# Optimization experiments

Measured on AMD Instinct MI355X. Metric: run time of the kernel, lower is better.

Reference implementation:

```python
import jax, jax.numpy as jnp
import numpy as np

B, T, C, H = 2, 2048, 1024, 16
D = C // H  # head dim = 64

def setup_inputs() -> dict:
    key = jax.random.key(0)
    k1, k2 = jax.random.split(key)
    x = jax.random.normal(k1, (B, T, C), dtype=jnp.float32)
    W_attn = jax.random.normal(k2, (3 * C, C), dtype=jnp.float32) * 0.02
    return {"x": x, "W_attn": W_attn}

def reference(x, W_attn):
    Bx, Tx, Cx = x.shape
    qkv = jnp.einsum('btc,fc->btf', x, W_attn)  # fused QKV projection (bias=False)
    q, k, v = jnp.split(qkv, 3, axis=-1)
    # [B, H, T, D]
    q = q.reshape(Bx, Tx, H, D).transpose(0, 2, 1, 3)
    k = k.reshape(Bx, Tx, H, D).transpose(0, 2, 1, 3)
    v = v.reshape(Bx, Tx, H, D).transpose(0, 2, 1, 3)
    scale = 1.0 / jnp.sqrt(jnp.asarray(D, dtype=q.dtype))
    scores = jnp.einsum('bhqd,bhkd->bhqk', q, k) * scale  # [B,H,T,T]
    causal = jnp.tril(jnp.ones((Tx, Tx), dtype=bool))
    scores = jnp.where(causal[None, None], scores, jnp.asarray(-jnp.inf, dtype=scores.dtype))
    attn = jax.nn.softmax(scores, axis=-1)
    y = jnp.einsum('bhqk,bhkd->bhqd', attn, v)
    y = y.transpose(0, 2, 1, 3).reshape(Bx, Tx, Cx)  # merge heads; dropout=0 at eval
    return y
```

## Files before the change

### kernel.cpp

```cpp
#include <hip/hip_runtime.h>
#include <hip/hip_bf16.h>

#define Bn 2
#define Tn 2048
#define Cn 1024
#define Hn 16
#define Dn 64
#define Mdim 4096
#define Ndim 3072
#define Kdim 1024

typedef unsigned short u16;
typedef __attribute__((ext_vector_type(8))) short bf16x8;
typedef __attribute__((ext_vector_type(4))) float f32x4;

__device__ __forceinline__ u16 f2bf(float v) {
    unsigned int x = __builtin_bit_cast(unsigned int, v);
    unsigned int r = (x + 0x7fffu + ((x >> 16) & 1u)) >> 16;
    return (u16)r;
}

__device__ __forceinline__ unsigned int pack2(float a, float b) {
    return (unsigned int)f2bf(a) | ((unsigned int)f2bf(b) << 16);
}

__device__ __forceinline__ unsigned int cvt_pk_bf16(float lo, float hi) {
    unsigned int r;
    asm("v_cvt_pk_bf16_f32 %0, %1, %2" : "=v"(r) : "v"(lo), "v"(hi));
    return r;
}

__device__ __forceinline__ void async16(const void* g, void* l) {
    __builtin_amdgcn_global_load_lds(
        (const __attribute__((address_space(1))) void*)g,
        (__attribute__((address_space(3))) void*)(unsigned int)(unsigned long long)l,
        16, 0, 0);
}

__device__ __forceinline__ int probe_inline(const unsigned int* __restrict__ X, int tid) {
    const int lane = tid & 63;
    int cnt = 0;
    #pragma unroll
    for (int i = 0; i < 8; i++) {
        unsigned int e = (X[lane * 8 + i] >> 7) & 0xFFu;
        cnt += (e >= 100u && e < 134u) ? 1 : 0;
    }
    #pragma unroll
    for (int off = 1; off < 64; off <<= 1) cnt += __shfl_xor(cnt, off);
    return cnt > 256 ? 1 : 0;
}

#define NXC ((size_t)Mdim * Kdim / 8)
#define NWC ((size_t)Ndim * Kdim / 8)

__global__ __launch_bounds__(256) void convert_in(
        const void* __restrict__ Xv, const void* __restrict__ Wv,
        u16* __restrict__ Xb, u16* __restrict__ Wb, int* __restrict__ flag) {
    const int isbf = probe_inline((const unsigned int*)Xv, threadIdx.x);
    if (blockIdx.x == 0 && threadIdx.x == 0) *flag = isbf;
    size_t i = (size_t)blockIdx.x * 256 + threadIdx.x;
    if (i >= NXC + NWC) return;
    const void* src; u16* dst; size_t off;
    if (i < NXC) { src = Xv; dst = Xb; off = i; }
    else         { src = Wv; dst = Wb; off = i - NXC; }
    if (isbf) {
        ((uint4*)dst)[off] = ((const uint4*)src)[off];
    } else {
        const float4* s = (const float4*)src + off * 2;
        float4 a = s[0], b = s[1];
        ((uint4*)dst)[off] = (uint4){pack2(a.x, a.y), pack2(a.z, a.w),
                                     pack2(b.x, b.y), pack2(b.z, b.w)};
    }
}

#define NTq (Kdim / 64)

#define PBAR() do { asm volatile("" ::: "memory"); \
                    __builtin_amdgcn_s_barrier();  \
                    asm volatile("" ::: "memory"); } while (0)
#define VMW(n) asm volatile("s_waitcnt vmcnt(" #n ")" ::: "memory")

#define QSTAGE_A(QIDX, BUF, KOFF) \
    async16(Xb + (size_t)(m0 + (QIDX) * 64 + srow) * Kdim + (KOFF) + gc, \
            &sA[BUF][(QIDX) * 4096 + w * 512])
#define QSTAGE_B(QIDX, BUF, KOFF) \
    async16(Wb + (size_t)(n0 + (QIDX) * 64 + srow) * Kdim + (KOFF) + gc, \
            &sB[BUF][(QIDX) * 4096 + w * 512])

#define RDA(MQ, BUF) do {                                                  \
    _Pragma("unroll")                                                      \
    for (int mt = 0; mt < 4; mt++) {                                       \
        const u16* p = &sA[BUF][(wm + (MQ) * 64 + mt * 16 + r16) * 64];    \
        af[mt][0] = *(const bf16x8*)(p + cx0);                             \
        af[mt][1] = *(const bf16x8*)(p + (cx0 ^ 32));                      \
    } } while (0)

#define RDB(NQ, BUF) do {                                                  \
    _Pragma("unroll")                                                      \
    for (int nt = 0; nt < 2; nt++) {                                       \
        const u16* p = &sB[BUF][(wn + (NQ) * 32 + nt * 16 + r16) * 64];    \
        bf[NQ][nt][0] = *(const bf16x8*)(p + cx0);                         \
        bf[NQ][nt][1] = *(const bf16x8*)(p + (cx0 ^ 32));                  \
    } } while (0)

#define MM(MQ, NQ) do {                                                    \
    __builtin_amdgcn_s_setprio(1);                                         \
    _Pragma("unroll")                                                      \
    for (int mt = 0; mt < 4; mt++)                                         \
        _Pragma("unroll")                                                  \
        for (int nt = 0; nt < 2; nt++) {                                   \
            acc[(MQ)*4+mt][(NQ)*2+nt] = __builtin_amdgcn_mfma_f32_16x16x32_bf16( \
                af[mt][0], bf[NQ][nt][0], acc[(MQ)*4+mt][(NQ)*2+nt], 0,0,0);     \
            acc[(MQ)*4+mt][(NQ)*2+nt] = __builtin_amdgcn_mfma_f32_16x16x32_bf16( \
                af[mt][1], bf[NQ][nt][1], acc[(MQ)*4+mt][(NQ)*2+nt], 0,0,0);     \
        }                                                                  \
    __builtin_amdgcn_s_setprio(0);                                         \
} while (0)

__global__ __launch_bounds__(512, 2) void qkv_gemm(
        const u16* __restrict__ Xb, const u16* __restrict__ Wb,
        u16* __restrict__ Q, u16* __restrict__ Kc, u16* __restrict__ Vt) {
    __shared__ __align__(16) u16 sA[2][256 * 64];
    __shared__ __align__(16) u16 sB[2][256 * 64];

    const int tid  = threadIdx.x;
    const int lane = tid & 63;
    const int w    = tid >> 6;
    const int quad = lane >> 4;
    const int r16  = lane & 15;
    const int wm   = (w >> 2) * 128;
    const int wn   = (w & 3) * 64;

    const int l0 = blockIdx.x;
    const int nl = (l0 & 7) * 24 + (l0 >> 3);
    const int m0 = (nl / 12) * 256;
    const int n0 = (nl % 12) * 256;

    const int lr   = lane >> 3;
    const int gc   = ((lane & 7) ^ lr) * 8;
    const int srow = w * 8 + lr;

    const int cx0 = (quad ^ (r16 & 7)) * 8;

    f32x4 acc[8][4];
    #pragma unroll
    for (int i = 0; i < 8; i++)
        #pragma unroll
        for (int j = 0; j < 4; j++)
            acc[i][j] = (f32x4){0.f, 0.f, 0.f, 0.f};

    bf16x8 af[4][2];
    bf16x8 bf[2][2][2];

    #pragma unroll
    for (int q = 0; q < 4; q++) { QSTAGE_A(q, 0, 0); QSTAGE_B(q, 0, 0); }
    VMW(0);
    PBAR();

    int koff = 0;
    for (int kt = 0; kt < NTq; kt++) {
        const int cur = kt & 1, nxt = cur ^ 1;
        const bool pf = (kt + 1 < NTq);
        const int kn = koff + 64;
        RDA(0, cur); RDB(0, cur);
        if (pf) { QSTAGE_B(0, nxt, kn); QSTAGE_B(1, nxt, kn); }
        PBAR(); MM(0, 0); PBAR();
        RDB(1, cur);
        if (pf) { QSTAGE_B(2, nxt, kn); QSTAGE_B(3, nxt, kn); }
        VMW(4); PBAR(); MM(0, 1); PBAR();
        RDA(1, cur);
        if (pf) { QSTAGE_A(0, nxt, kn); QSTAGE_A(2, nxt, kn); }
        PBAR(); MM(1, 1); PBAR();
        if (pf) { QSTAGE_A(1, nxt, kn); QSTAGE_A(3, nxt, kn); }
        VMW(2); PBAR(); MM(1, 0); PBAR();
        koff = kn;
    }

    const int sect = n0 >> 10;
    #pragma unroll
    for (int mq = 0; mq < 2; mq++)
    #pragma unroll
    for (int mt = 0; mt < 4; mt++)
    #pragma unroll
    for (int nq = 0; nq < 2; nq++)
    #pragma unroll
    for (int nt = 0; nt < 2; nt++) {
        f32x4 v4 = acc[mq * 4 + mt][nq * 2 + nt];
        const int mBase = m0 + wm + mq * 64 + mt * 16 + quad * 4;
        const int f = n0 + wn + nq * 32 + nt * 16 + r16;
        const int b = mBase >> 11;
        const int t0 = mBase & 2047;
        const int h = (f >> 6) & 15;
        const int d = f & 63;
        const int bh = b * Hn + h;
        if (sect == 0) {
            #pragma unroll
            for (int r = 0; r < 4; r++)
                Q[((size_t)(bh * Tn + t0 + r)) * Dn + d] = f2bf(v4[r] * 0.125f);
        } else if (sect == 1) {
            #pragma unroll
            for (int r = 0; r < 4; r++)
                Kc[((size_t)(bh * Tn + t0 + r)) * Dn + d] = f2bf(v4[r]);
        } else {
            ushort4 pk4 = {f2bf(v4[0]), f2bf(v4[1]), f2bf(v4[2]), f2bf(v4[3])};
            *(ushort4*)(Vt + ((size_t)(bh * Dn + d)) * Tn + t0) = pk4;
        }
    }
}


#define SWZ(R, C) ((R) * 64 + (((C) * 8) ^ (((R) & 7) << 3)))

#define STAGE(KB, BUF) do {                                                    \
    const int kbase_ = (KB) * 64;                                              \
    if (w < 4) {                                                               \
        _Pragma("unroll")                                                      \
        for (int i = 0; i < 2; i++) {                                          \
            const int seg = w * 2 + i;             \
            async16(Kc + qkBase + (size_t)(kbase_ + seg * 8 + rl) * Dn + gc8,  \
                    &sK[BUF][seg * 512]);                                      \
        }                                                                      \
    } else {                                                                   \
        _Pragma("unroll")                                                      \
        for (int i = 0; i < 2; i++) {                                          \
            const int seg = (w - 4) * 2 + i;     \
            async16(Vt + vBase + (size_t)(seg * 8 + rl) * Tn + kbase_ + gc8,   \
                    &sV[BUF][seg * 512]);                                      \
        }                                                                      \
    }                                                                          \
} while (0)

#define COMPUTE(KB, BUF) do {                                                  \
    const int kbase_ = (KB) * 64;                                              \
    const bool diag_ = ((KB) == nkb_w - 1);                                    \
    bf16x8 kf[4][2], vf[4][2];                                                 \
    _Pragma("unroll")                                                          \
    for (int nt = 0; nt < 4; nt++) {                                           \
        kf[nt][0] = *(const bf16x8*)&sK[BUF][SWZ(nt * 16 + r16, quad)];        \
        kf[nt][1] = *(const bf16x8*)&sK[BUF][SWZ(nt * 16 + r16, 4 + quad)];    \
    }                                                                          \
    _Pragma("unroll")                                                          \
    for (int dt = 0; dt < 4; dt++) {                                           \
        vf[dt][0] = *(const bf16x8*)&sV[BUF][SWZ(dt * 16 + r16, quad)];        \
        vf[dt][1] = *(const bf16x8*)&sV[BUF][SWZ(dt * 16 + r16, 4 + quad)];    \
    }                                                                          \
    _Pragma("unroll")                                                          \
    for (int mt = 0; mt < 2; mt++) {                                           \
        f32x4 s[4];                                                            \
        __builtin_amdgcn_s_setprio(1);                                         \
        _Pragma("unroll")                                                      \
        for (int nt = 0; nt < 4; nt++) {                                       \
            f32x4 z = (f32x4){-8.f, -8.f, -8.f, -8.f};                         \
            z = __builtin_amdgcn_mfma_f32_16x16x32_bf16(kf[nt][0], aq[mt][0], z, 0, 0, 0); \
            z = __builtin_amdgcn_mfma_f32_16x16x32_bf16(kf[nt][1], aq[mt][1], z, 0, 0, 0); \
            s[nt] = z;                                                         \
        }                                                                      \
        __builtin_amdgcn_s_setprio(0);                                         \
        if (diag_) {                                                           \
            const int query = qw0 + mt * 16 + r16;                             \
            _Pragma("unroll")                                                  \
            for (int nt = 0; nt < 4; nt++)                                     \
                _Pragma("unroll")                                              \
                for (int r = 0; r < 4; r++) {                                  \
                    int key = kbase_ + nt * 16 + quad * 4 + r;                 \
                    if (key > query) s[nt][r] = -1e30f;                        \
                }                                                              \
        }                                                                      \
        unsigned int pk[4][2];                                                 \
        _Pragma("unroll")                                                      \
        for (int nt = 0; nt < 4; nt++) {                                       \
            float p0 = __expf(s[nt][0]);                                       \
            float p1 = __expf(s[nt][1]);                                       \
            float p2 = __expf(s[nt][2]);                                       \
            float p3 = __expf(s[nt][3]);                                       \
            lacc[mt] += (p0 + p1) + (p2 + p3);                                 \
            pk[nt][0] = cvt_pk_bf16(p0, p1);                                   \
            pk[nt][1] = cvt_pk_bf16(p2, p3);                                   \
        }                                                                      \
        _Pragma("unroll")                                                      \
        for (int kc = 0; kc < 2; kc++) {                                       \
            int4 bq;                                                           \
            _Pragma("unroll")                                                  \
            for (int h = 0; h < 2; h++) {                                      \
                unsigned int a = pk[kc * 2 + 0][h];                            \
                unsigned int b = pk[kc * 2 + 1][h];                            \
                auto t = __builtin_amdgcn_permlane32_swap(a, b, false, false); \
                auto u = __builtin_amdgcn_permlane16_swap(t[0], t[1], false, false); \
                ((unsigned int*)&bq)[0 + h] = u[0];                            \
                ((unsigned int*)&bq)[2 + h] = u[1];                            \
            }                                                                  \
            bf16x8 bqv = __builtin_bit_cast(bf16x8, bq);                       \
            __builtin_amdgcn_s_setprio(1);                                     \
            _Pragma("unroll")                                                  \
            for (int dt = 0; dt < 4; dt++)                                     \
                o[mt][dt] = __builtin_amdgcn_mfma_f32_16x16x32_bf16(           \
                    vf[dt][kc], bqv, o[mt][dt], 0, 0, 0);                      \
            __builtin_amdgcn_s_setprio(0);                                     \
        }                                                                      \
    }                                                                          \
} while (0)

__global__ __launch_bounds__(512, 2) void attn(
        const u16* __restrict__ Q, const u16* __restrict__ Kc,
        const u16* __restrict__ Vt, void* __restrict__ Y,
        const int* __restrict__ flag) {
    __shared__ __align__(16) u16 sK[4][4096];
    __shared__ __align__(16) u16 sV[4][4096];

    const int isbf = *flag;
    const int tid  = threadIdx.x;
    const int lane = tid & 63;
    const int w    = tid >> 6;
    const int ws   = w & 3;
    const int quad = lane >> 4;
    const int r16  = lane & 15;
    const int bid  = blockIdx.x;
    const int bh   = bid & (Bn * Hn - 1);
    const int p    = bid >> 5;
    const int qt_w = (w < 4) ? (15 - p) : p;
    const int qw0  = qt_w * 128 + ws * 32;
    const size_t qkBase = (size_t)bh * Tn * Dn;
    const size_t vBase  = (size_t)bh * Dn * Tn;

    const int rl  = lane >> 3;
    const int gc8 = (((lane & 7) ^ rl)) * 8;

    bf16x8 aq[2][2];
    #pragma unroll
    for (int mt = 0; mt < 2; mt++) {
        const u16* qp = Q + qkBase + (size_t)(qw0 + mt * 16 + r16) * Dn;
        aq[mt][0] = *(const bf16x8*)(qp + quad * 8);
        aq[mt][1] = *(const bf16x8*)(qp + 32 + quad * 8);
    }

    float lacc[2] = {0.f, 0.f};
    f32x4 o[2][4];
    #pragma unroll
    for (int mt = 0; mt < 2; mt++)
        #pragma unroll
        for (int dt = 0; dt < 4; dt++) o[mt][dt] = (f32x4){0.f, 0.f, 0.f, 0.f};

    const int nkb_w = 2 * qt_w + 1 + (ws >> 1);
    const int kbmax = 31 - 2 * p;

    STAGE(0, 0);
    STAGE(1, 1);
    VMW(2);
    PBAR();

    for (int kb = 0; kb <= kbmax; kb++) {
        if (kb + 2 <= kbmax) { STAGE(kb + 2, (kb + 2) & 3); VMW(2); }
        else                 { VMW(0); }
        PBAR();
        if (kb < nkb_w) COMPUTE(kb, kb & 3);
    }

    const int b = bh >> 4, h = bh & 15;
    #pragma unroll
    for (int mt = 0; mt < 2; mt++) {
        float den = lacc[mt];
        den += __shfl_xor(den, 16);
        den += __shfl_xor(den, 32);
        float rden = 1.f / fmaxf(den, 1e-30f);
        int t = qw0 + mt * 16 + r16;
        #pragma unroll
        for (int dt = 0; dt < 4; dt++) {
            float v0 = o[mt][dt][0] * rden;
            float v1 = o[mt][dt][1] * rden;
            float v2 = o[mt][dt][2] * rden;
            float v3 = o[mt][dt][3] * rden;
            int c = h * Dn + dt * 16 + quad * 4;
            size_t idx = ((size_t)(b * Tn + t)) * Cn + c;
            if (isbf) {
                ushort4 pk4 = {f2bf(v0), f2bf(v1), f2bf(v2), f2bf(v3)};
                *(ushort4*)((u16*)Y + idx) = pk4;
            } else {
                float4 f4 = {v0, v1, v2, v3};
                *(float4*)((float*)Y + idx) = f4;
            }
        }
    }
}

extern "C" void kernel_launch(void* const* d_in, const int* in_sizes, int n_in,
                              void* d_out, int out_size, void* d_ws, size_t ws_size,
                              hipStream_t stream) {
    const void* X = d_in[0];
    const void* W = d_in[1];
    void* Y = d_out;

    const size_t per = (size_t)Bn * Hn * Tn * Dn;
    int* flag = (int*)d_ws;
    u16* Q  = (u16*)((char*)d_ws + 256);
    u16* Kc = Q + per;
    u16* Vt = Kc + per;
    u16* Xb = Vt + per;
    u16* Wb = Xb + (size_t)Mdim * Kdim;

    {
        const size_t nch = NXC + NWC;
        convert_in<<<dim3((unsigned)((nch + 255) / 256)), 256, 0, stream>>>(X, W, Xb, Wb, flag);
    }
    qkv_gemm<<<dim3((Mdim / 256) * (Ndim / 256)), 512, 0, stream>>>(Xb, Wb, Q, Kc, Vt);
    attn<<<dim3(Bn * Hn * (Tn / 256)), 512, 0, stream>>>(Q, Kc, Vt, Y, flag);
}
```

Measured before the change: 148.0 us.

## Serialize dense and sparse query tiles per block so all warps share work

Previously half the warps handled the long (diagonal-far) query tile and half the short one, so the short-tile warps idled while K/V blocks for the long tile streamed in. Now all 8 warps process 16 query rows of the long tile first, write its output, then reuse the same pipeline for the short tile over a fixed 34-step loop. This balances per-warp MFMA work and halves per-warp accumulator registers, at the cost of staging the short tile's K/V blocks a second time and a smaller M per MFMA tile.

```diff
diff --git a/kernel.cpp b/kernel.cpp
--- a/kernel.cpp
+++ b/kernel.cpp
@@ -211,28 +211,28 @@
 
 #define SWZ(R, C) ((R) * 64 + (((C) * 8) ^ (((R) & 7) << 3)))
 
-#define STAGE(KB, BUF) do {                                                    \
+#define ASTAGE(KB, BUF) do {                                                   \
     const int kbase_ = (KB) * 64;                                              \
     if (w < 4) {                                                               \
         _Pragma("unroll")                                                      \
-        for (int i = 0; i < 2; i++) {                                          \
-            const int seg = w * 2 + i;             \
+        for (int i_ = 0; i_ < 2; i_++) {                                       \
+            const int seg = w * 2 + i_;            \
             async16(Kc + qkBase + (size_t)(kbase_ + seg * 8 + rl) * Dn + gc8,  \
                     &sK[BUF][seg * 512]);                                      \
         }                                                                      \
     } else {                                                                   \
         _Pragma("unroll")                                                      \
-        for (int i = 0; i < 2; i++) {                                          \
-            const int seg = (w - 4) * 2 + i;     \
+        for (int i_ = 0; i_ < 2; i_++) {                                       \
+            const int seg = (w - 4) * 2 + i_;    \
             async16(Vt + vBase + (size_t)(seg * 8 + rl) * Tn + kbase_ + gc8,   \
                     &sV[BUF][seg * 512]);                                      \
         }                                                                      \
     }                                                                          \
 } while (0)
 
-#define COMPUTE(KB, BUF) do {                                                  \
+#define ACOMP(KB, BUF, QW0, NKB, AQ) do {                                      \
     const int kbase_ = (KB) * 64;                                              \
-    const bool diag_ = ((KB) == nkb_w - 1);                                    \
+    const bool diag_ = ((KB) == (NKB) - 1);                                    \
     bf16x8 kf[4][2], vf[4][2];                                                 \
     _Pragma("unroll")                                                          \
     for (int nt = 0; nt < 4; nt++) {                                           \
@@ -244,58 +244,79 @@
         vf[dt][0] = *(const bf16x8*)&sV[BUF][SWZ(dt * 16 + r16, quad)];        \
         vf[dt][1] = *(const bf16x8*)&sV[BUF][SWZ(dt * 16 + r16, 4 + quad)];    \
     }                                                                          \
-    _Pragma("unroll")                                                          \
-    for (int mt = 0; mt < 2; mt++) {                                           \
-        f32x4 s[4];                                                            \
+    f32x4 s[4];                                                                \
+    __builtin_amdgcn_s_setprio(1);                                             \
+    _Pragma("unroll")                                                          \
+    for (int nt = 0; nt < 4; nt++) {                                           \
+        f32x4 z = (f32x4){-8.f, -8.f, -8.f, -8.f};                             \
+        z = __builtin_amdgcn_mfma_f32_16x16x32_bf16(kf[nt][0], AQ[0], z, 0, 0, 0); \
+        z = __builtin_amdgcn_mfma_f32_16x16x32_bf16(kf[nt][1], AQ[1], z, 0, 0, 0); \
+        s[nt] = z;                                                             \
+    }                                                                          \
+    __builtin_amdgcn_s_setprio(0);                                             \
+    if (diag_) {                                                               \
+        const int query = (QW0) + r16;                                         \
+        _Pragma("unroll")                                                      \
+        for (int nt = 0; nt < 4; nt++)                                         \
+            _Pragma("unroll")                                                  \
+            for (int r = 0; r < 4; r++) {                                      \
+                int key = kbase_ + nt * 16 + quad * 4 + r;                     \
+                if (key > query) s[nt][r] = -1e30f;                            \
+            }                                                                  \
+    }                                                                          \
+    unsigned int pk[4][2];                                                     \
+    _Pragma("unroll")                                                          \
+    for (int nt = 0; nt < 4; nt++) {                                           \
+        float p0 = __expf(s[nt][0]);                                           \
+        float p1 = __expf(s[nt][1]);                                           \
+        float p2 = __expf(s[nt][2]);                                           \
+        float p3 = __expf(s[nt][3]);                                           \
+        lacc += (p0 + p1) + (p2 + p3);                                         \
+        pk[nt][0] = cvt_pk_bf16(p0, p1);                                       \
+        pk[nt][1] = cvt_pk_bf16(p2, p3);                                       \
+    }                                                                          \
+    _Pragma("unroll")                                                          \
+    for (int kc = 0; kc < 2; kc++) {                                           \
+        int4 bq;                                                               \
+        _Pragma("unroll")                                                      \
+        for (int h_ = 0; h_ < 2; h_++) {                                       \
+            unsigned int a = pk[kc * 2 + 0][h_];                               \
+            unsigned int b = pk[kc * 2 + 1][h_];                               \
+            auto t = __builtin_amdgcn_permlane32_swap(a, b, false, false);     \
+            auto u = __builtin_amdgcn_permlane16_swap(t[0], t[1], false, false); \
+            ((unsigned int*)&bq)[0 + h_] = u[0];                               \
+            ((unsigned int*)&bq)[2 + h_] = u[1];                               \
+        }                                                                      \
+        bf16x8 bqv = __builtin_bit_cast(bf16x8, bq);                           \
         __builtin_amdgcn_s_setprio(1);                                         \
         _Pragma("unroll")                                                      \
-        for (int nt = 0; nt < 4; nt++) {                                       \
-            f32x4 z = (f32x4){-8.f, -8.f, -8.f, -8.f};                         \
-            z = __builtin_amdgcn_mfma_f32_16x16x32_bf16(kf[nt][0], aq[mt][0], z, 0, 0, 0); \
-            z = __builtin_amdgcn_mfma_f32_16x16x32_bf16(kf[nt][1], aq[mt][1], z, 0, 0, 0); \
-            s[nt] = z;                                                         \
-        }                                                                      \
+        for (int dt = 0; dt < 4; dt++)                                         \
+            o[dt] = __builtin_amdgcn_mfma_f32_16x16x32_bf16(                   \
+                vf[dt][kc], bqv, o[dt], 0, 0, 0);                              \
         __builtin_amdgcn_s_setprio(0);                                         \
-        if (diag_) {                                                           \
-            const int query = qw0 + mt * 16 + r16;                             \
-            _Pragma("unroll")                                                  \
-            for (int nt = 0; nt < 4; nt++)                                     \
-                _Pragma("unroll")                                              \
-                for (int r = 0; r < 4; r++) {                                  \
-                    int key = kbase_ + nt * 16 + quad * 4 + r;                 \
-                    if (key > query) s[nt][r] = -1e30f;                        \
-                }                                                              \
-        }                                                                      \
-        unsigned int pk[4][2];                                                 \
-        _Pragma("unroll")                                                      \
-        for (int nt = 0; nt < 4; nt++) {                                       \
-            float p0 = __expf(s[nt][0]);                                       \
-            float p1 = __expf(s[nt][1]);                                       \
-            float p2 = __expf(s[nt][2]);                                       \
-            float p3 = __expf(s[nt][3]);                                       \
-            lacc[mt] += (p0 + p1) + (p2 + p3);                                 \
-            pk[nt][0] = cvt_pk_bf16(p0, p1);                                   \
-            pk[nt][1] = cvt_pk_bf16(p2, p3);                                   \
-        }                                                                      \
-        _Pragma("unroll")                                                      \
-        for (int kc = 0; kc < 2; kc++) {                                       \
-            int4 bq;                                                           \
-            _Pragma("unroll")                                                  \
-            for (int h = 0; h < 2; h++) {                                      \
-                unsigned int a = pk[kc * 2 + 0][h];                            \
-                unsigned int b = pk[kc * 2 + 1][h];                            \
-                auto t = __builtin_amdgcn_permlane32_swap(a, b, false, false); \
-                auto u = __builtin_amdgcn_permlane16_swap(t[0], t[1], false, false); \
-                ((unsigned int*)&bq)[0 + h] = u[0];                            \
-                ((unsigned int*)&bq)[2 + h] = u[1];                            \
-            }                                                                  \
-            bf16x8 bqv = __builtin_bit_cast(bf16x8, bq);                       \
-            __builtin_amdgcn_s_setprio(1);                                     \
-            _Pragma("unroll")                                                  \
-            for (int dt = 0; dt < 4; dt++)                                     \
-                o[mt][dt] = __builtin_amdgcn_mfma_f32_16x16x32_bf16(           \
-                    vf[dt][kc], bqv, o[mt][dt], 0, 0, 0);                      \
-            __builtin_amdgcn_s_setprio(0);                                     \
+    }                                                                          \
+} while (0)
+
+#define AEPI(QW0) do {                                                         \
+    float den = lacc;                                                          \
+    den += __shfl_xor(den, 16);                                                \
+    den += __shfl_xor(den, 32);                                                \
+    float rden = 1.f / fmaxf(den, 1e-30f);                                     \
+    int t = (QW0) + r16;                                                       \
+    _Pragma("unroll")                                                          \
+    for (int dt = 0; dt < 4; dt++) {                                           \
+        float v0 = o[dt][0] * rden;                                            \
+        float v1 = o[dt][1] * rden;                                            \
+        float v2 = o[dt][2] * rden;                                            \
+        float v3 = o[dt][3] * rden;                                            \
+        int c = hh * Dn + dt * 16 + quad * 4;                                  \
+        size_t idx = ((size_t)(bb * Tn + t)) * Cn + c;                         \
+        if (isbf) {                                                            \
+            ushort4 pk4 = {f2bf(v0), f2bf(v1), f2bf(v2), f2bf(v3)};            \
+            *(ushort4*)((u16*)Y + idx) = pk4;                                  \
+        } else {                                                               \
+            float4 f4 = {v0, v1, v2, v3};                                      \
+            *(float4*)((float*)Y + idx) = f4;                                  \
         }                                                                      \
     }                                                                          \
 } while (0)
@@ -311,75 +332,69 @@
     const int tid  = threadIdx.x;
     const int lane = tid & 63;
     const int w    = tid >> 6;
-    const int ws   = w & 3;
     const int quad = lane >> 4;
     const int r16  = lane & 15;
     const int bid  = blockIdx.x;
     const int bh   = bid & (Bn * Hn - 1);
     const int p    = bid >> 5;
-    const int qt_w = (w < 4) ? (15 - p) : p;
-    const int qw0  = qt_w * 128 + ws * 32;
+    const int qtd  = 15 - p, qts = p;
+    const int nd   = 2 * qtd + 2;
+    const int qd0  = qtd * 128 + w * 16;
+    const int qs0  = qts * 128 + w * 16;
+    const int nkb_d = 2 * qtd + 1 + (w >> 2);
+    const int nkb_s = 2 * qts + 1 + (w >> 2);
     const size_t qkBase = (size_t)bh * Tn * Dn;
     const size_t vBase  = (size_t)bh * Dn * Tn;
+    const int bb = bh >> 4, hh = bh & 15;
 
     const int rl  = lane >> 3;
     const int gc8 = (((lane & 7) ^ rl)) * 8;
 
-    bf16x8 aq[2][2];
-    #pragma unroll
-    for (int mt = 0; mt < 2; mt++) {
-        const u16* qp = Q + qkBase + (size_t)(qw0 + mt * 16 + r16) * Dn;
-        aq[mt][0] = *(const bf16x8*)(qp + quad * 8);
-        aq[mt][1] = *(const bf16x8*)(qp + 32 + quad * 8);
-    }
-
-    float lacc[2] = {0.f, 0.f};
-    f32x4 o[2][4];
-    #pragma unroll
-    for (int mt = 0; mt < 2; mt++)
-        #pragma unroll
-        for (int dt = 0; dt < 4; dt++) o[mt][dt] = (f32x4){0.f, 0.f, 0.f, 0.f};
-
-    const int nkb_w = 2 * qt_w + 1 + (ws >> 1);
-    const int kbmax = 31 - 2 * p;
-
-    STAGE(0, 0);
-    STAGE(1, 1);
+    bf16x8 aqd[2], aqs[2];
+    {
+        const u16* qp = Q + qkBase + (size_t)(qd0 + r16) * Dn;
+        aqd[0] = *(const bf16x8*)(qp + quad * 8);
+        aqd[1] = *(const bf16x8*)(qp + 32 + quad * 8);
+        const u16* qs = Q + qkBase + (size_t)(qs0 + r16) * Dn;
+        aqs[0] = *(const bf16x8*)(qs + quad * 8);
+        aqs[1] = *(const bf16x8*)(qs + 32 + quad * 8);
+    }
+
+    float lacc = 0.f;
+    f32x4 o[4];
+    #pragma unroll
+    for (int dt = 0; dt < 4; dt++) o[dt] = (f32x4){0.f, 0.f, 0.f, 0.f};
+
+    ASTAGE(0, 0);
+    ASTAGE(1, 1);
     VMW(2);
     PBAR();
 
-    for (int kb = 0; kb <= kbmax; kb++) {
-        if (kb + 2 <= kbmax) { STAGE(kb + 2, (kb + 2) & 3); VMW(2); }
-        else                 { VMW(0); }
+    for (int i = 0; i < 34; i++) {
+        if (i + 2 < 34) {
+            const int j = i + 2;
+            const int kbj = (j < nd) ? j : (j - nd);
+            ASTAGE(kbj, j & 3);
+            VMW(2);
+        } else {
+            VMW(0);
+        }
         PBAR();
-        if (kb < nkb_w) COMPUTE(kb, kb & 3);
-    }
-
-    const int b = bh >> 4, h = bh & 15;
-    #pragma unroll
-    for (int mt = 0; mt < 2; mt++) {
-        float den = lacc[mt];
-        den += __shfl_xor(den, 16);
-        den += __shfl_xor(den, 32);
-        float rden = 1.f / fmaxf(den, 1e-30f);
-        int t = qw0 + mt * 16 + r16;
-        #pragma unroll
-        for (int dt = 0; dt < 4; dt++) {
-            float v0 = o[mt][dt][0] * rden;
-            float v1 = o[mt][dt][1] * rden;
-            float v2 = o[mt][dt][2] * rden;
-            float v3 = o[mt][dt][3] * rden;
-            int c = h * Dn + dt * 16 + quad * 4;
-            size_t idx = ((size_t)(b * Tn + t)) * Cn + c;
-            if (isbf) {
-                ushort4 pk4 = {f2bf(v0), f2bf(v1), f2bf(v2), f2bf(v3)};
-                *(ushort4*)((u16*)Y + idx) = pk4;
-            } else {
-                float4 f4 = {v0, v1, v2, v3};
-                *(float4*)((float*)Y + idx) = f4;
+        if (i < nd) {
+            if (i < nkb_d) ACOMP(i, i & 3, qd0, nkb_d, aqd);
+            if (i == nd - 1) {
+                AEPI(qd0);
+                lacc = 0.f;
+                #pragma unroll
+                for (int dt = 0; dt < 4; dt++) o[dt] = (f32x4){0.f, 0.f, 0.f, 0.f};
             }
+        } else {
+            const int kb = i - nd;
+            if (kb < nkb_s) ACOMP(kb, i & 3, qs0, nkb_s, aqs);
         }
     }
+
+    AEPI(qs0);
 }
 
 extern "C" void kernel_launch(void* const* d_in, const int* in_sizes, int n_in,
```

Result: no change. 149.7 us (+1.2%).

## Split paired attention blocks into separate 256-thread blocks per query tile

Applied to the files above, without the earlier changes.

Before, each 512-thread block handled two query tiles, a heavy one and a light one, so causal work was balanced inside the block while both halves shared K/V staging. Now each 256-thread block handles one 128-row query tile, launched with twice the blocks and heavy tiles ordered first, and loads only the key blocks that tile needs. This aims to stop the light half from idling while it waits for staging of the heavy half's keys, and to give more, smaller blocks for scheduling. In exchange each warp issues twice as many async loads per stage and K/V reuse across the paired tiles is lost.

```diff
diff --git a/kernel.cpp b/kernel.cpp
--- a/kernel.cpp
+++ b/kernel.cpp
@@ -211,28 +211,28 @@
 
 #define SWZ(R, C) ((R) * 64 + (((C) * 8) ^ (((R) & 7) << 3)))
 
-#define STAGE(KB, BUF) do {                                                    \
+#define ASTG(KB, BUF) do {                                                     \
     const int kbase_ = (KB) * 64;                                              \
-    if (w < 4) {                                                               \
+    if (w < 2) {                                                               \
         _Pragma("unroll")                                                      \
-        for (int i = 0; i < 2; i++) {                                          \
-            const int seg = w * 2 + i;             \
+        for (int i_ = 0; i_ < 4; i_++) {                                       \
+            const int seg = w * 4 + i_;            \
             async16(Kc + qkBase + (size_t)(kbase_ + seg * 8 + rl) * Dn + gc8,  \
                     &sK[BUF][seg * 512]);                                      \
         }                                                                      \
     } else {                                                                   \
         _Pragma("unroll")                                                      \
-        for (int i = 0; i < 2; i++) {                                          \
-            const int seg = (w - 4) * 2 + i;     \
+        for (int i_ = 0; i_ < 4; i_++) {                                       \
+            const int seg = (w - 2) * 4 + i_;    \
             async16(Vt + vBase + (size_t)(seg * 8 + rl) * Tn + kbase_ + gc8,   \
                     &sV[BUF][seg * 512]);                                      \
         }                                                                      \
     }                                                                          \
 } while (0)
 
-#define COMPUTE(KB, BUF) do {                                                  \
+#define ACOMP(KB, BUF) do {                                                    \
     const int kbase_ = (KB) * 64;                                              \
-    const bool diag_ = ((KB) == nkb_w - 1);                                    \
+    const bool diag_ = ((KB) == nkb - 1);                                      \
     bf16x8 kf[4][2], vf[4][2];                                                 \
     _Pragma("unroll")                                                          \
     for (int nt = 0; nt < 4; nt++) {                                           \
@@ -281,13 +281,13 @@
         for (int kc = 0; kc < 2; kc++) {                                       \
             int4 bq;                                                           \
             _Pragma("unroll")                                                  \
-            for (int h = 0; h < 2; h++) {                                      \
-                unsigned int a = pk[kc * 2 + 0][h];                            \
-                unsigned int b = pk[kc * 2 + 1][h];                            \
+            for (int h_ = 0; h_ < 2; h_++) {                                   \
+                unsigned int a = pk[kc * 2 + 0][h_];                           \
+                unsigned int b = pk[kc * 2 + 1][h_];                           \
                 auto t = __builtin_amdgcn_permlane32_swap(a, b, false, false); \
                 auto u = __builtin_amdgcn_permlane16_swap(t[0], t[1], false, false); \
-                ((unsigned int*)&bq)[0 + h] = u[0];                            \
-                ((unsigned int*)&bq)[2 + h] = u[1];                            \
+                ((unsigned int*)&bq)[0 + h_] = u[0];                           \
+                ((unsigned int*)&bq)[2 + h_] = u[1];                           \
             }                                                                  \
             bf16x8 bqv = __builtin_bit_cast(bf16x8, bq);                       \
             __builtin_amdgcn_s_setprio(1);                                     \
@@ -300,7 +300,7 @@
     }                                                                          \
 } while (0)
 
-__global__ __launch_bounds__(512, 2) void attn(
+__global__ __launch_bounds__(256, 2) void attn(
         const u16* __restrict__ Q, const u16* __restrict__ Kc,
         const u16* __restrict__ Vt, void* __restrict__ Y,
         const int* __restrict__ flag) {
@@ -311,16 +311,19 @@
     const int tid  = threadIdx.x;
     const int lane = tid & 63;
     const int w    = tid >> 6;
-    const int ws   = w & 3;
     const int quad = lane >> 4;
     const int r16  = lane & 15;
     const int bid  = blockIdx.x;
     const int bh   = bid & (Bn * Hn - 1);
-    const int p    = bid >> 5;
-    const int qt_w = (w < 4) ? (15 - p) : p;
-    const int qw0  = qt_w * 128 + ws * 32;
+    const int half = bid >> 8;
+    const int j    = (bid & 255) >> 5;
+    const int qt   = half ? j : (15 - j);
+    const int qw0  = qt * 128 + w * 32;
+    const int nt   = 2 * qt + 2;
+    const int nkb  = 2 * qt + 1 + (w >> 1);
     const size_t qkBase = (size_t)bh * Tn * Dn;
     const size_t vBase  = (size_t)bh * Dn * Tn;
+    const int bb = bh >> 4, hh = bh & 15;
 
     const int rl  = lane >> 3;
     const int gc8 = (((lane & 7) ^ rl)) * 8;
@@ -340,22 +343,19 @@
         #pragma unroll
         for (int dt = 0; dt < 4; dt++) o[mt][dt] = (f32x4){0.f, 0.f, 0.f, 0.f};
 
-    const int nkb_w = 2 * qt_w + 1 + (ws >> 1);
-    const int kbmax = 31 - 2 * p;
-
-    STAGE(0, 0);
-    STAGE(1, 1);
-    VMW(2);
+    ASTG(0, 0);
+    ASTG(1, 1);
+    VMW(4);
     PBAR();
 
-    for (int kb = 0; kb <= kbmax; kb++) {
-        if (kb + 2 <= kbmax) { STAGE(kb + 2, (kb + 2) & 3); VMW(2); }
+    for (int i = 0; i < nt; i++) {
+        if (i + 2 < nt)      { ASTG(i + 2, (i + 2) & 3); VMW(8); }
+        else if (i + 1 < nt) { VMW(4); }
         else                 { VMW(0); }
         PBAR();
-        if (kb < nkb_w) COMPUTE(kb, kb & 3);
-    }
-
-    const int b = bh >> 4, h = bh & 15;
+        if (i < nkb) ACOMP(i, i & 3);
+    }
+
     #pragma unroll
     for (int mt = 0; mt < 2; mt++) {
         float den = lacc[mt];
@@ -369,8 +369,8 @@
             float v1 = o[mt][dt][1] * rden;
             float v2 = o[mt][dt][2] * rden;
             float v3 = o[mt][dt][3] * rden;
-            int c = h * Dn + dt * 16 + quad * 4;
-            size_t idx = ((size_t)(b * Tn + t)) * Cn + c;
+            int c = hh * Dn + dt * 16 + quad * 4;
+            size_t idx = ((size_t)(bb * Tn + t)) * Cn + c;
             if (isbf) {
                 ushort4 pk4 = {f2bf(v0), f2bf(v1), f2bf(v2), f2bf(v3)};
                 *(ushort4*)((u16*)Y + idx) = pk4;
@@ -402,5 +402,5 @@
         convert_in<<<dim3((unsigned)((nch + 255) / 256)), 256, 0, stream>>>(X, W, Xb, Wb, flag);
     }
     qkv_gemm<<<dim3((Mdim / 256) * (Ndim / 256)), 512, 0, stream>>>(Xb, Wb, Q, Kc, Vt);
-    attn<<<dim3(Bn * Hn * (Tn / 256)), 512, 0, stream>>>(Q, Kc, Vt, Y, flag);
-}
+    attn<<<dim3(Bn * Hn * (Tn / 128)), 256, 0, stream>>>(Q, Kc, Vt, Y, flag);
+}
```

Measured after the change: 147.5 us. Within noise of the previous version (-0.3%).
